# Performance work log

Hardware: AMD Instinct MI355X
Metric: run time of the kernel (lower is better)

## Reference

```python
import jax, jax.numpy as jnp
import numpy as np

N_SCALES = 3
BASE_SIGMA = 0.1
SCALES = jnp.asarray([BASE_SIGMA * 2.0 ** i for i in range(N_SCALES)], dtype=jnp.float32)


def setup_inputs() -> dict:
    key = jax.random.key(0)
    k_x, k_pos, k_tp, k_w1, k_b1, k_w2, k_b2 = jax.random.split(key, 7)
    B, C, T = 16, 306, 4000
    M = 128
    x = jax.random.normal(k_x, (B, C, T), dtype=jnp.float32)
    positions = jax.random.normal(k_pos, (B, C, 2), dtype=jnp.float32)
    target_positions = jax.random.normal(k_tp, (M, 2), dtype=jnp.float32)
    # nn.Linear(3, 32) / nn.Linear(32, 1) params (kaiming-uniform-ish init)
    lim1 = 1.0 / np.sqrt(3.0)
    w1 = jax.random.uniform(k_w1, (3, 32), jnp.float32, -lim1, lim1)
    b1 = jax.random.uniform(k_b1, (32,), jnp.float32, -lim1, lim1)
    lim2 = 1.0 / np.sqrt(32.0)
    w2 = jax.random.uniform(k_w2, (32, 1), jnp.float32, -lim2, lim2)
    b2 = jax.random.uniform(k_b2, (1,), jnp.float32, -lim2, lim2)
    return {"x": x, "positions": positions, "target_positions": target_positions,
            "w1": w1, "b1": b1, "w2": w2, "b2": b2}


def reference(x, positions, target_positions, w1, b1, w2, b2):
    # squared euclidean distances [B, C, M]
    diff = positions[:, :, None, :] - target_positions[None, None, :, :]
    d2 = jnp.sum(diff * diff, axis=-1)
    # multi-scale Gaussian kernels, stacked on last axis -> [B, C, M, n_scales]
    inv = 1.0 / (2.0 * SCALES ** 2)  # [n_scales]
    scale_weights = jnp.exp(-d2[..., None] * inv)
    # tiny 2-layer MLP gate: (3 -> 32 -> 1)
    h = jax.nn.relu(scale_weights @ w1 + b1)  # [B, C, M, 32]
    w = (h @ w2 + b2)[..., 0]                 # [B, C, M]
    # normalize over channel dim
    w = w / (jnp.sum(w, axis=1, keepdims=True) + 1e-8)
    # weighted channel aggregation -> [B, M, T]
    return jnp.einsum('bct,bcm->bmt', x, w)
```

## Files before the change

### kernel.cpp

```cpp
#include <hip/hip_runtime.h>

#define B_ 16
#define C_ 306
#define T_ 4000
#define M_ 128

typedef short bf16x8 __attribute__((ext_vector_type(8)));
typedef float f32x4 __attribute__((ext_vector_type(4)));

#define WF_PER_B 81920

__global__ __launch_bounds__(320)
void gate_kernel(const float* __restrict__ positions,
                 const float* __restrict__ target,
                 const float* __restrict__ w1,
                 const float* __restrict__ b1,
                 const float* __restrict__ w2,
                 const float* __restrict__ b2,
                 unsigned short* __restrict__ wf,
                 float* __restrict__ scale) {
    const int b  = blockIdx.x >> 5;
    const int mg = blockIdx.x & 31;
    const int tid = threadIdx.x;

    __shared__ float s_w1[96], s_b1[32], s_w2[32];
    __shared__ float s_b2;
    __shared__ float s_tgt[8];
    __shared__ float s_part[4][5];
    __shared__ unsigned short s_frag[40 * 72];

    if (tid < 96) s_w1[tid] = w1[tid];
    if (tid < 32) { s_b1[tid] = b1[tid]; s_w2[tid] = w2[tid]; }
    if (tid == 256) s_b2 = b2[0];
    if (tid >= 312) s_tgt[tid - 312] = target[mg * 8 + (tid - 312)];
    __syncthreads();

    float px = 0.0f, py = 0.0f;
    if (tid < C_) {
        px = positions[(b * C_ + tid) * 2 + 0];
        py = positions[(b * C_ + tid) * 2 + 1];
    }

    float wv_[4];
#pragma unroll
    for (int mi = 0; mi < 4; ++mi) {
        float w = 0.0f;
        if (tid < C_) {
            const float dx = px - s_tgt[mi * 2 + 0];
            const float dy = py - s_tgt[mi * 2 + 1];
            const float d2 = dx * dx + dy * dy;
            const float s2 = __expf(-d2 * 3.125f);
            const float q  = s2 * s2;
            const float s1 = q * q;
            const float r  = s1 * s1;
            const float s0 = r * r;
            float acc = s_b2;
#pragma unroll
            for (int j = 0; j < 32; ++j) {
                float h = fmaf(s0, s_w1[j],
                          fmaf(s1, s_w1[32 + j],
                          fmaf(s2, s_w1[64 + j], s_b1[j])));
                acc = fmaf(fmaxf(h, 0.0f), s_w2[j], acc);
            }
            w = acc;
        }
        wv_[mi] = w;
    }

#pragma unroll
    for (int mi = 0; mi < 4; ++mi) {
        float s = wv_[mi];
#pragma unroll
        for (int off = 32; off > 0; off >>= 1) s += __shfl_down(s, off, 64);
        if ((tid & 63) == 0) s_part[mi][tid >> 6] = s;
    }

    const int chunk = tid >> 3;
    const int slot  = tid & 7;
#pragma unroll
    for (int mi = 0; mi < 4; ++mi) {
        const float w = wv_[mi];
        const unsigned int u = __float_as_uint(w);
        const unsigned short h = (unsigned short)(u >> 16);
        const float lof = w - __uint_as_float(u & 0xffff0000u);
        const unsigned short l = (unsigned short)(__float_as_uint(lof) >> 16);
        s_frag[chunk * 72 + mi * 16 + 0 + slot] = h;
        s_frag[chunk * 72 + mi * 16 + 8 + slot] = l;
    }
    __syncthreads();

    if (tid < 4) {
        float tot = s_part[tid][0] + s_part[tid][1] + s_part[tid][2]
                  + s_part[tid][3] + s_part[tid][4];
        scale[b * M_ + mg * 4 + tid] = 1.0f / (tot + 1e-8f);
    }

    {
        const int ch = tid >> 3;
        const int g  = tid & 7;
        const uint4 v = *(const uint4*)(s_frag + ch * 72 + g * 8);
        unsigned short* dst = wf + (size_t)b * WF_PER_B
                            + (size_t)ch * 2048 + mg * 64 + g * 8;
        *(uint4*)dst = v;
    }
}

#define RS4 320

__global__ __launch_bounds__(512, 4)
void merge_gemm(const float* __restrict__ x,
                const unsigned short* __restrict__ wf,
                const float* __restrict__ scale,
                float* __restrict__ out) {
    const int t0 = blockIdx.x * 64;
    const int b  = blockIdx.y;
    const int tid  = threadIdx.x;
    const int lane = tid & 63;
    const int wv   = tid >> 6;
    const int tquad = lane >> 4;
    const int tsub  = lane & 15;

    __shared__ __align__(16) unsigned int sX[64 * RS4];

    const float* xb = x + (size_t)b * C_ * T_;
    const unsigned short* wfB = wf + (size_t)b * WF_PER_B;

    const int mw  = (wv & 3) * 32;
    const int tw2 = (wv >> 2) * 32;

    auto loadW = [&](int k, bf16x8* ah_, bf16x8* al_) {
#pragma unroll
        for (int mi = 0; mi < 2; ++mi) {
            const size_t aoff = ((size_t)(k * 4 + tquad) * 128
                               + (mw + mi * 16 + tsub)) * 16;
            ah_[mi] = *(const bf16x8*)(wfB + aoff);
            al_[mi] = *(const bf16x8*)(wfB + aoff + 8);
        }
    };

    const int cp = tid & 31;
    const int TQ = tid >> 5;
    const float* xcol = xb + min(t0 + TQ * 4, T_ - 4);

    bf16x8 ah[2], al[2];

    float4 va[5], vb[5];
#pragma unroll
    for (int j = 0; j < 5; ++j) {
        const int c = (j * 32 + cp) * 2;
        va[j] = *(const float4*)(xcol + (size_t)min(c,     C_ - 1) * T_);
        vb[j] = *(const float4*)(xcol + (size_t)min(c + 1, C_ - 1) * T_);
    }
    loadW(0, ah, al);

#pragma unroll
    for (int j = 0; j < 5; ++j) {
        const int p = j * 32 + cp;
        const float* fa = (const float*)&va[j];
        const float* fb = (const float*)&vb[j];
#pragma unroll
        for (int tt = 0; tt < 4; ++tt) {
            const int t = TQ * 4 + tt;
            const int q = t * RS4 + (p ^ ((t & 7) << 2));
            const unsigned int ua = __float_as_uint(fa[tt]);
            const unsigned int ub = __float_as_uint(fb[tt]);
            const float la = fa[tt] - __uint_as_float(ua & 0xffff0000u);
            const float lb = fb[tt] - __uint_as_float(ub & 0xffff0000u);
            sX[q]       = __builtin_amdgcn_perm(ub, ua, 0x07060302u);
            sX[q + 160] = __builtin_amdgcn_perm(__float_as_uint(lb),
                                                __float_as_uint(la),
                                                0x07060302u);
        }
    }
    __syncthreads();

    f32x4 acc[2][2];
#pragma unroll
    for (int i = 0; i < 2; ++i)
#pragma unroll
        for (int j = 0; j < 2; ++j) acc[i][j] = (f32x4){0.f, 0.f, 0.f, 0.f};

    int rbase[2], tswz[2];
#pragma unroll
    for (int ti = 0; ti < 2; ++ti) {
        const int t = tw2 + ti * 16 + tsub;
        rbase[ti] = t * RS4;
        tswz[ti]  = (t & 7) << 2;
    }

#pragma unroll
    for (int k = 0; k < 10; ++k) {
        bf16x8 bh[2], bl[2];
#pragma unroll
        for (int ti = 0; ti < 2; ++ti) {
            const int q = rbase[ti] + ((k * 16 + tquad * 4) ^ tswz[ti]);
            bh[ti] = *(const bf16x8*)(&sX[q]);
            bl[ti] = *(const bf16x8*)(&sX[q + 160]);
        }

#pragma unroll
        for (int mi = 0; mi < 2; ++mi)
#pragma unroll
            for (int ti = 0; ti < 2; ++ti)
                acc[mi][ti] = __builtin_amdgcn_mfma_f32_16x16x32_bf16(
                    ah[mi], bh[ti], acc[mi][ti], 0, 0, 0);
#pragma unroll
        for (int mi = 0; mi < 2; ++mi)
#pragma unroll
            for (int ti = 0; ti < 2; ++ti)
                acc[mi][ti] = __builtin_amdgcn_mfma_f32_16x16x32_bf16(
                    ah[mi], bl[ti], acc[mi][ti], 0, 0, 0);
#pragma unroll
        for (int mi = 0; mi < 2; ++mi)
#pragma unroll
            for (int ti = 0; ti < 2; ++ti)
                acc[mi][ti] = __builtin_amdgcn_mfma_f32_16x16x32_bf16(
                    al[mi], bh[ti], acc[mi][ti], 0, 0, 0);

        if (k < 9) loadW(k + 1, ah, al);
    }

#pragma unroll
    for (int mi = 0; mi < 2; ++mi) {
        const int mbase = mw + mi * 16 + tquad * 4;
        const float4 sc = *(const float4*)(scale + b * M_ + mbase);
        float* op = out + ((size_t)b * M_ + mbase) * T_;
#pragma unroll
        for (int ti = 0; ti < 2; ++ti) {
            const int tg = t0 + tw2 + ti * 16 + tsub;
            if (tg < T_) {
                op[(size_t)0 * T_ + tg] = acc[mi][ti][0] * sc.x;
                op[(size_t)1 * T_ + tg] = acc[mi][ti][1] * sc.y;
                op[(size_t)2 * T_ + tg] = acc[mi][ti][2] * sc.z;
                op[(size_t)3 * T_ + tg] = acc[mi][ti][3] * sc.w;
            }
        }
    }
}

extern "C" void kernel_launch(void* const* d_in, const int* in_sizes, int n_in,
                              void* d_out, int out_size, void* d_ws, size_t ws_size,
                              hipStream_t stream) {
    const float* x         = (const float*)d_in[0];
    const float* positions = (const float*)d_in[1];
    const float* target    = (const float*)d_in[2];
    const float* w1        = (const float*)d_in[3];
    const float* b1        = (const float*)d_in[4];
    const float* w2        = (const float*)d_in[5];
    const float* b2        = (const float*)d_in[6];
    float* out = (float*)d_out;

    float* scale = (float*)d_ws;
    unsigned short* wf = (unsigned short*)(scale + B_ * M_);

    gate_kernel<<<B_ * 32, 320, 0, stream>>>(positions, target, w1, b1, w2, b2,
                                             wf, scale);

    dim3 grid((T_ + 63) / 64, B_);
    merge_gemm<<<grid, 512, 0, stream>>>(x, wf, scale, out);
}
```

Measured before the change: 156.3 us.

## Widen merge GEMM time tile and double-buffer channel chunks through LDS

The merge GEMM tile grows from 64 to 256 time steps per block, so each block reuses the gate-weight fragments across more columns. Channels are now processed in five chunks of 64 through two shared-memory buffers, with the next chunk's global loads issued before the current chunk's MFMAs and packed afterwards. This replaces the old single upfront load and split of all channels. The aim is to overlap global x loads with matrix work and cut redundant weight loads. In exchange there are fewer blocks (grid of 16x16), larger per-thread accumulator state and lower occupancy (launch bounds 512,2), which may leave part of the GPU idle.

```diff
diff --git a/kernel.cpp b/kernel.cpp
--- a/kernel.cpp
+++ b/kernel.cpp
@@ -105,14 +105,15 @@
     }
 }
 
-#define RS4 320
-
-__global__ __launch_bounds__(512, 4)
+#define TW 256
+#define PL 8192
+
+__global__ __launch_bounds__(512, 2)
 void merge_gemm(const float* __restrict__ x,
                 const unsigned short* __restrict__ wf,
                 const float* __restrict__ scale,
                 float* __restrict__ out) {
-    const int t0 = blockIdx.x * 64;
+    const int t0 = blockIdx.x * TW;
     const int b  = blockIdx.y;
     const int tid  = threadIdx.x;
     const int lane = tid & 63;
@@ -120,104 +121,130 @@
     const int tquad = lane >> 4;
     const int tsub  = lane & 15;
 
-    __shared__ __align__(16) unsigned int sX[64 * RS4];
+    __shared__ __align__(16) unsigned int sX[2][2][PL];
 
     const float* xb = x + (size_t)b * C_ * T_;
     const unsigned short* wfB = wf + (size_t)b * WF_PER_B;
 
     const int mw  = (wv & 3) * 32;
-    const int tw2 = (wv >> 2) * 32;
-
-    auto loadW = [&](int k, bf16x8* ah_, bf16x8* al_) {
-#pragma unroll
-        for (int mi = 0; mi < 2; ++mi) {
-            const size_t aoff = ((size_t)(k * 4 + tquad) * 128
-                               + (mw + mi * 16 + tsub)) * 16;
-            ah_[mi] = *(const bf16x8*)(wfB + aoff);
-            al_[mi] = *(const bf16x8*)(wfB + aoff + 8);
+    const int twv = (wv >> 2) * 128;
+
+    const int cp = tid >> 5;
+    const int TQ = tid & 31;
+
+    auto loadX = [&](int k, float4 (&A)[2][2], float4 (&B)[2][2]) {
+#pragma unroll
+        for (int h = 0; h < 2; ++h) {
+            const int p  = cp + 16 * h;
+            const int c0 = k * 64 + 2 * p;
+#pragma unroll
+            for (int s = 0; s < 2; ++s) {
+                const int tq = TQ + 32 * s;
+                const float* col = xb + min(t0 + tq * 4, T_ - 4);
+                A[h][s] = *(const float4*)(col + (size_t)min(c0,     C_ - 1) * T_);
+                B[h][s] = *(const float4*)(col + (size_t)min(c0 + 1, C_ - 1) * T_);
+            }
         }
     };
-
-    const int cp = tid & 31;
-    const int TQ = tid >> 5;
-    const float* xcol = xb + min(t0 + TQ * 4, T_ - 4);
-
-    bf16x8 ah[2], al[2];
-
-    float4 va[5], vb[5];
-#pragma unroll
-    for (int j = 0; j < 5; ++j) {
-        const int c = (j * 32 + cp) * 2;
-        va[j] = *(const float4*)(xcol + (size_t)min(c,     C_ - 1) * T_);
-        vb[j] = *(const float4*)(xcol + (size_t)min(c + 1, C_ - 1) * T_);
-    }
-    loadW(0, ah, al);
-
-#pragma unroll
-    for (int j = 0; j < 5; ++j) {
-        const int p = j * 32 + cp;
-        const float* fa = (const float*)&va[j];
-        const float* fb = (const float*)&vb[j];
-#pragma unroll
-        for (int tt = 0; tt < 4; ++tt) {
-            const int t = TQ * 4 + tt;
-            const int q = t * RS4 + (p ^ ((t & 7) << 2));
-            const unsigned int ua = __float_as_uint(fa[tt]);
-            const unsigned int ub = __float_as_uint(fb[tt]);
-            const float la = fa[tt] - __uint_as_float(ua & 0xffff0000u);
-            const float lb = fb[tt] - __uint_as_float(ub & 0xffff0000u);
-            sX[q]       = __builtin_amdgcn_perm(ub, ua, 0x07060302u);
-            sX[q + 160] = __builtin_amdgcn_perm(__float_as_uint(lb),
-                                                __float_as_uint(la),
-                                                0x07060302u);
-        }
-    }
-    __syncthreads();
-
-    f32x4 acc[2][2];
+    auto packX = [&](const float4 (&A)[2][2], const float4 (&B)[2][2], int buf) {
+#pragma unroll
+        for (int h = 0; h < 2; ++h) {
+            const int p = cp + 16 * h;
+#pragma unroll
+            for (int s = 0; s < 2; ++s) {
+                const int tq = TQ + 32 * s;
+                const int swz = (tq & 7) << 2;
+                const float* fa = (const float*)&A[h][s];
+                const float* fb = (const float*)&B[h][s];
+#pragma unroll
+                for (int tt = 0; tt < 4; ++tt) {
+                    const int t = tq * 4 + tt;
+                    const int addr = t * 32 + (p ^ swz);
+                    const unsigned int ua = __float_as_uint(fa[tt]);
+                    const unsigned int ub = __float_as_uint(fb[tt]);
+                    const float la = fa[tt] - __uint_as_float(ua & 0xffff0000u);
+                    const float lb = fb[tt] - __uint_as_float(ub & 0xffff0000u);
+                    sX[buf][0][addr] = __builtin_amdgcn_perm(ub, ua, 0x07060302u);
+                    sX[buf][1][addr] = __builtin_amdgcn_perm(__float_as_uint(lb),
+                                                             __float_as_uint(la),
+                                                             0x07060302u);
+                }
+            }
+        }
+    };
+    auto loadW = [&](int k, bf16x8 (&ah_)[2][2], bf16x8 (&al_)[2][2]) {
+#pragma unroll
+        for (int kk = 0; kk < 2; ++kk)
+#pragma unroll
+            for (int mi = 0; mi < 2; ++mi) {
+                const size_t aoff = ((size_t)(k * 8 + kk * 4 + tquad) * 128
+                                   + (mw + mi * 16 + tsub)) * 16;
+                ah_[kk][mi] = *(const bf16x8*)(wfB + aoff);
+                al_[kk][mi] = *(const bf16x8*)(wfB + aoff + 8);
+            }
+    };
+
+    f32x4 acc[2][8];
 #pragma unroll
     for (int i = 0; i < 2; ++i)
 #pragma unroll
-        for (int j = 0; j < 2; ++j) acc[i][j] = (f32x4){0.f, 0.f, 0.f, 0.f};
-
-    int rbase[2], tswz[2];
-#pragma unroll
-    for (int ti = 0; ti < 2; ++ti) {
-        const int t = tw2 + ti * 16 + tsub;
-        rbase[ti] = t * RS4;
-        tswz[ti]  = (t & 7) << 2;
-    }
-
-#pragma unroll
-    for (int k = 0; k < 10; ++k) {
-        bf16x8 bh[2], bl[2];
-#pragma unroll
-        for (int ti = 0; ti < 2; ++ti) {
-            const int q = rbase[ti] + ((k * 16 + tquad * 4) ^ tswz[ti]);
-            bh[ti] = *(const bf16x8*)(&sX[q]);
-            bl[ti] = *(const bf16x8*)(&sX[q + 160]);
-        }
-
-#pragma unroll
-        for (int mi = 0; mi < 2; ++mi)
-#pragma unroll
-            for (int ti = 0; ti < 2; ++ti)
-                acc[mi][ti] = __builtin_amdgcn_mfma_f32_16x16x32_bf16(
-                    ah[mi], bh[ti], acc[mi][ti], 0, 0, 0);
-#pragma unroll
-        for (int mi = 0; mi < 2; ++mi)
-#pragma unroll
-            for (int ti = 0; ti < 2; ++ti)
-                acc[mi][ti] = __builtin_amdgcn_mfma_f32_16x16x32_bf16(
-                    ah[mi], bl[ti], acc[mi][ti], 0, 0, 0);
-#pragma unroll
-        for (int mi = 0; mi < 2; ++mi)
-#pragma unroll
-            for (int ti = 0; ti < 2; ++ti)
-                acc[mi][ti] = __builtin_amdgcn_mfma_f32_16x16x32_bf16(
-                    al[mi], bh[ti], acc[mi][ti], 0, 0, 0);
-
-        if (k < 9) loadW(k + 1, ah, al);
+        for (int j = 0; j < 8; ++j) acc[i][j] = (f32x4){0.f, 0.f, 0.f, 0.f};
+
+    bf16x8 ah[2][2], al[2][2];
+    {
+        float4 A0[2][2], B0[2][2];
+        loadX(0, A0, B0);
+        loadW(0, ah, al);
+        packX(A0, B0, 0);
+    }
+    asm volatile("s_waitcnt lgkmcnt(0)" ::: "memory");
+    __builtin_amdgcn_s_barrier();
+    asm volatile("" ::: "memory");
+
+    int rbase[8], tswz[8];
+#pragma unroll
+    for (int ti = 0; ti < 8; ++ti) {
+        const int t = twv + ti * 16 + tsub;
+        rbase[ti] = t * 32;
+        tswz[ti]  = ((t >> 2) & 7) << 2;
+    }
+
+#pragma unroll
+    for (int k = 0; k < 5; ++k) {
+        float4 An[2][2], Bn[2][2];
+        if (k < 4) loadX(k + 1, An, Bn);
+
+        const int buf = k & 1;
+#pragma unroll
+        for (int kk = 0; kk < 2; ++kk) {
+            const int Q = kk * 16 + tquad * 4;
+#pragma unroll
+            for (int ti = 0; ti < 8; ++ti) {
+                const int a = rbase[ti] + (Q ^ tswz[ti]);
+                const bf16x8 bh = *(const bf16x8*)(&sX[buf][0][a]);
+                const bf16x8 bl = *(const bf16x8*)(&sX[buf][1][a]);
+#pragma unroll
+                for (int mi = 0; mi < 2; ++mi)
+                    acc[mi][ti] = __builtin_amdgcn_mfma_f32_16x16x32_bf16(
+                        ah[kk][mi], bh, acc[mi][ti], 0, 0, 0);
+#pragma unroll
+                for (int mi = 0; mi < 2; ++mi)
+                    acc[mi][ti] = __builtin_amdgcn_mfma_f32_16x16x32_bf16(
+                        ah[kk][mi], bl, acc[mi][ti], 0, 0, 0);
+#pragma unroll
+                for (int mi = 0; mi < 2; ++mi)
+                    acc[mi][ti] = __builtin_amdgcn_mfma_f32_16x16x32_bf16(
+                        al[kk][mi], bh, acc[mi][ti], 0, 0, 0);
+            }
+        }
+
+        if (k < 4) {
+            loadW(k + 1, ah, al);
+            packX(An, Bn, buf ^ 1);
+            asm volatile("s_waitcnt lgkmcnt(0)" ::: "memory");
+            __builtin_amdgcn_s_barrier();
+            asm volatile("" ::: "memory");
+        }
     }
 
 #pragma unroll
@@ -226,8 +253,8 @@
         const float4 sc = *(const float4*)(scale + b * M_ + mbase);
         float* op = out + ((size_t)b * M_ + mbase) * T_;
 #pragma unroll
-        for (int ti = 0; ti < 2; ++ti) {
-            const int tg = t0 + tw2 + ti * 16 + tsub;
+        for (int ti = 0; ti < 8; ++ti) {
+            const int tg = t0 + twv + ti * 16 + tsub;
             if (tg < T_) {
                 op[(size_t)0 * T_ + tg] = acc[mi][ti][0] * sc.x;
                 op[(size_t)1 * T_ + tg] = acc[mi][ti][1] * sc.y;
@@ -256,6 +283,6 @@
     gate_kernel<<<B_ * 32, 320, 0, stream>>>(positions, target, w1, b1, w2, b2,
                                              wf, scale);
 
-    dim3 grid((T_ + 63) / 64, B_);
+    dim3 grid((T_ + TW - 1) / TW, B_);
     merge_gemm<<<grid, 512, 0, stream>>>(x, wf, scale, out);
 }
```

Result: faster. 144.8 us (median of 2 runs) (-7.4%).
